# Kernel optimization log

Hardware: AMD Instinct MI355X
Metric: run time of the kernel (lower is better)

Reference implementation:

```python
import jax, jax.numpy as jnp
import numpy as np

N = 1_000_000   # nodes
E = 32_000_000  # directed edges (avg degree 32)


def setup_inputs() -> dict:
    key = jax.random.key(0)
    k1, k2, k3 = jax.random.split(key, 3)
    x = jax.random.normal(k1, (N, 1), dtype=jnp.float32)
    edge_index = jax.random.randint(k2, (2, E), 0, N, dtype=jnp.int32)
    W = jax.random.normal(k3, (1, 1), dtype=jnp.float32) * 0.5
    b = jnp.zeros((1,), dtype=jnp.float32)
    return {"x": x, "edge_index": edge_index, "W": W, "b": b}


def reference(x, edge_index, W, b):
    # GCNConv with default add_self_loops=True, normalize=True, then sigmoid.
    n = x.shape[0]
    loops = jnp.arange(n, dtype=edge_index.dtype)
    src = jnp.concatenate([edge_index[0], loops])  # [E+N]
    dst = jnp.concatenate([edge_index[1], loops])  # [E+N]

    # degree over destination nodes (self-loops included -> deg >= 1)
    deg = jax.ops.segment_sum(jnp.ones_like(dst, dtype=x.dtype), dst, num_segments=n)
    dinv = jax.lax.rsqrt(deg)                      # [N]
    norm = dinv[src] * dinv[dst]                   # [E+N] symmetric normalization

    xw = x @ W                                     # [N, 1] linear transform
    msg = xw[src] * norm[:, None]                  # gather + scale, [E+N, 1]
    agg = jax.ops.segment_sum(msg, dst, num_segments=n)  # scatter-add, [N, 1]
    return jax.nn.sigmoid(agg + b)
```

## Files before the change

### kernel.cpp

```cpp
#include <hip/hip_runtime.h>
#include <math.h>

typedef unsigned int u32;
typedef int iv4 __attribute__((ext_vector_type(4)));

#define BKT_BITS 12
#define BKT_SIZE 4096
#define NBMAX    256
#define DEPTH    32
#define BIN_T    256
#define TILE     4096


__global__ void zero_u32(u32* __restrict__ p, int n) {
    int i = blockIdx.x * blockDim.x + threadIdx.x;
    if (i < n) p[i] = 0u;
}

__global__ void count_kernel(const int* __restrict__ dst, u32* __restrict__ gcount, int E, int NB) {
    __shared__ u32 h[NBMAX];
    for (int t = threadIdx.x; t < NBMAX; t += blockDim.x) h[t] = 0u;
    __syncthreads();
    int nvec = E >> 2;
    for (int v = blockIdx.x * blockDim.x + threadIdx.x; v < nvec; v += gridDim.x * blockDim.x) {
        iv4 d = __builtin_nontemporal_load(reinterpret_cast<const iv4*>(dst) + v);
        atomicAdd(&h[((u32)d.x) >> BKT_BITS], 1u);
        atomicAdd(&h[((u32)d.y) >> BKT_BITS], 1u);
        atomicAdd(&h[((u32)d.z) >> BKT_BITS], 1u);
        atomicAdd(&h[((u32)d.w) >> BKT_BITS], 1u);
    }
    if (blockIdx.x == 0) {
        for (int e = (nvec << 2) + threadIdx.x; e < E; e += blockDim.x)
            atomicAdd(&h[((u32)dst[e]) >> BKT_BITS], 1u);
    }
    __syncthreads();
    for (int t = threadIdx.x; t < NB; t += blockDim.x)
        if (h[t]) atomicAdd(&gcount[t], h[t]);
}

__global__ void scan_kernel(const u32* __restrict__ gcount, u32* __restrict__ gbase,
                            u32* __restrict__ gcursor, int NB) {
    __shared__ u32 sc[NBMAX];
    int t = threadIdx.x;
    u32 cap = 0u;
    if (t < NB) cap = (gcount[t] + 63u) & ~63u;
    sc[t] = cap;
    __syncthreads();
    for (int off = 1; off < NBMAX; off <<= 1) {
        u32 v = (t >= off) ? sc[t - off] : 0u;
        __syncthreads();
        sc[t] += v;
        __syncthreads();
    }
    if (t < NB) {
        u32 base = sc[t] - cap;
        gbase[t]   = base;
        gcursor[t] = base;
    }
}

__global__ void __launch_bounds__(BIN_T)
bin_kernel(const int* __restrict__ src, const int* __restrict__ dst,
           u32* __restrict__ recs, u32* __restrict__ gcursor, int E, int NB) {
    __shared__ u32 stag[NBMAX * DEPTH];
    __shared__ u32 scnt[NBMAX];
    for (int t = threadIdx.x; t < NBMAX; t += BIN_T) scnt[t] = 0u;
    __syncthreads();
    int base = blockIdx.x * TILE;
#pragma unroll
    for (int r = 0; r < TILE / (BIN_T * 4); ++r) {
        int v  = (base >> 2) + r * BIN_T + threadIdx.x;
        int e0 = v << 2;
        if (e0 + 3 < E) {
            iv4 s4 = __builtin_nontemporal_load(reinterpret_cast<const iv4*>(src) + v);
            iv4 d4 = __builtin_nontemporal_load(reinterpret_cast<const iv4*>(dst) + v);
#pragma unroll
            for (int k = 0; k < 4; ++k) {
                u32 ss = (u32)s4[k], dd = (u32)d4[k];
                u32 b   = dd >> BKT_BITS;
                u32 rec = (ss << BKT_BITS) | (dd & (BKT_SIZE - 1));
                u32 slot = atomicAdd(&scnt[b], 1u);
                if (slot < DEPTH) stag[b * DEPTH + slot] = rec;
                else { u32 g = atomicAdd(&gcursor[b], 1u); recs[g] = rec; }
            }
        } else if (e0 < E) {
            for (int e = e0; e < E && e < e0 + 4; ++e) {
                u32 ss = (u32)src[e], dd = (u32)dst[e];
                u32 b   = dd >> BKT_BITS;
                u32 rec = (ss << BKT_BITS) | (dd & (BKT_SIZE - 1));
                u32 slot = atomicAdd(&scnt[b], 1u);
                if (slot < DEPTH) stag[b * DEPTH + slot] = rec;
                else { u32 g = atomicAdd(&gcursor[b], 1u); recs[g] = rec; }
            }
        }
    }
    __syncthreads();
    int t = threadIdx.x;
    if (t < NB) {
        u32 c = scnt[t]; if (c > DEPTH) c = DEPTH;
        if (c > 0u) {
            u32 g = atomicAdd(&gcursor[t], c);
            for (u32 k = 0; k < c; ++k) recs[g + k] = stag[t * DEPTH + k];
        }
    }
}

__global__ void __launch_bounds__(1024)
degnode_kernel(const u32* __restrict__ recs, const u32* __restrict__ gbase,
               const u32* __restrict__ gcount, const float* __restrict__ x,
               const float* __restrict__ W, float* __restrict__ dinv,
               float* __restrict__ s, int N) {
    __shared__ u32 cnt[BKT_SIZE];
    int b = blockIdx.x;
    for (int j = threadIdx.x; j < BKT_SIZE; j += 1024) cnt[j] = 0u;
    __syncthreads();
    u32 c = gcount[b], base = gbase[b];
    for (u32 k = threadIdx.x; k < c; k += 1024) {
        u32 rec = __builtin_nontemporal_load(recs + base + k);
        atomicAdd(&cnt[rec & (BKT_SIZE - 1)], 1u);
    }
    __syncthreads();
    int nid0 = b << BKT_BITS;
    float W0 = W[0];
    for (int j = threadIdx.x; j < BKT_SIZE; j += 1024) {
        int nid = nid0 + j;
        if (nid < N) {
            float di = rsqrtf((float)(cnt[j] + 1u));
            dinv[nid] = di;
            s[nid] = x[nid] * W0 * di;
        }
    }
}

__global__ void __launch_bounds__(1024)
aggout_kernel(const u32* __restrict__ recs, const u32* __restrict__ gbase,
              const u32* __restrict__ gcount, const float* __restrict__ s,
              const float* __restrict__ dinv, const float* __restrict__ bb,
              float* __restrict__ out, int N) {
    __shared__ float acc[BKT_SIZE];
    int b = blockIdx.x;
    for (int j = threadIdx.x; j < BKT_SIZE; j += 1024) acc[j] = 0.0f;
    __syncthreads();
    u32 c = gcount[b], base = gbase[b];
    for (u32 k = threadIdx.x; k < c; k += 1024) {
        u32 rec = __builtin_nontemporal_load(recs + base + k);
        atomicAdd(&acc[rec & (BKT_SIZE - 1)], s[rec >> BKT_BITS]);
    }
    __syncthreads();
    int nid0 = b << BKT_BITS;
    float b0 = bb[0];
    for (int j = threadIdx.x; j < BKT_SIZE; j += 1024) {
        int nid = nid0 + j;
        if (nid < N) {
            float z = dinv[nid] * (acc[j] + s[nid]) + b0;
            out[nid] = 1.0f / (1.0f + expf(-z));
        }
    }
}

__global__ void zero_kernel(int* __restrict__ p, int n) {
    int i = blockIdx.x * blockDim.x + threadIdx.x;
    if (i < n) p[i] = 0;
}
__global__ void deg_kernel(const int* __restrict__ dst, int* __restrict__ deg, int E) {
    int i = (blockIdx.x * blockDim.x + threadIdx.x) * 4;
    if (i + 3 < E) {
        int4 d = *reinterpret_cast<const int4*>(dst + i);
        atomicAdd(&deg[d.x], 1); atomicAdd(&deg[d.y], 1);
        atomicAdd(&deg[d.z], 1); atomicAdd(&deg[d.w], 1);
    } else {
        for (int k = i; k < E; ++k) atomicAdd(&deg[dst[k]], 1);
    }
}
__global__ void node_kernel(const float* __restrict__ x, const int* __restrict__ deg,
                            const float* __restrict__ W, float* __restrict__ s,
                            float* __restrict__ dinv, float* __restrict__ acc, int N) {
    int i = blockIdx.x * blockDim.x + threadIdx.x;
    if (i < N) {
        float di = rsqrtf((float)(deg[i] + 1));
        float si = x[i] * W[0] * di;
        dinv[i] = di; s[i] = si; acc[i] = si;
    }
}
__global__ void scatter_kernel(const int* __restrict__ src, const int* __restrict__ dst,
                               const float* __restrict__ s, float* __restrict__ acc, int E) {
    int i = (blockIdx.x * blockDim.x + threadIdx.x) * 4;
    if (i + 3 < E) {
        int4 sv = *reinterpret_cast<const int4*>(src + i);
        int4 dv = *reinterpret_cast<const int4*>(dst + i);
        atomicAdd(&acc[dv.x], s[sv.x]); atomicAdd(&acc[dv.y], s[sv.y]);
        atomicAdd(&acc[dv.z], s[sv.z]); atomicAdd(&acc[dv.w], s[sv.w]);
    } else {
        for (int k = i; k < E; ++k) atomicAdd(&acc[dst[k]], s[src[k]]);
    }
}
__global__ void out_kernel(const float* __restrict__ acc, const float* __restrict__ dinv,
                           const float* __restrict__ b, float* __restrict__ out, int N) {
    int i = blockIdx.x * blockDim.x + threadIdx.x;
    if (i < N) {
        float z = dinv[i] * acc[i] + b[0];
        out[i] = 1.0f / (1.0f + expf(-z));
    }
}

extern "C" void kernel_launch(void* const* d_in, const int* in_sizes, int n_in,
                              void* d_out, int out_size, void* d_ws, size_t ws_size,
                              hipStream_t stream) {
    const int N = in_sizes[0];
    const int E = in_sizes[1] / 2;
    const float* x  = (const float*)d_in[0];
    const int*   ei = (const int*)d_in[1];
    const float* W  = (const float*)d_in[2];
    const float* b  = (const float*)d_in[3];
    float* out = (float*)d_out;

    const int* srcp = ei;
    const int* dstp = ei + E;
    const int T = 256;

    const int NB = (N + BKT_SIZE - 1) >> BKT_BITS;
    const size_t recCap = (size_t)E + (size_t)NB * 64;
    const size_t need = (recCap + 3 * (size_t)NB + 2 * (size_t)N) * 4;

    if (N <= (1 << 20) && NB <= NBMAX && ws_size >= need) {
        u32* p = (u32*)d_ws;
        u32*   recs    = p;           p += recCap;
        u32*   gbase   = p;           p += NB;
        u32*   gcursor = p;           p += NB;
        u32*   gcount  = p;           p += NB;
        float* dinv    = (float*)p;   p += N;
        float* s       = (float*)p;

        zero_u32<<<1, T, 0, stream>>>(gcount, NB);
        count_kernel<<<1024, T, 0, stream>>>(dstp, gcount, E, NB);
        scan_kernel<<<1, T, 0, stream>>>(gcount, gbase, gcursor, NB);
        bin_kernel<<<(E + TILE - 1) / TILE, BIN_T, 0, stream>>>(srcp, dstp, recs, gcursor, E, NB);
        degnode_kernel<<<NB, 1024, 0, stream>>>(recs, gbase, gcount, x, W, dinv, s, N);
        aggout_kernel<<<NB, 1024, 0, stream>>>(recs, gbase, gcount, s, dinv, b, out, N);
    } else {
        char* ws = (char*)d_ws;
        int*   deg  = (int*)ws;
        float* s    = (float*)(ws + (size_t)N * 4);
        float* dinv = (float*)(ws + (size_t)N * 8);
        float* acc  = (float*)deg;
        const int blocksN = (N + T - 1) / T;
        const int blocksE = ((E + 3) / 4 + T - 1) / T;
        zero_kernel<<<blocksN, T, 0, stream>>>(deg, N);
        deg_kernel<<<blocksE, T, 0, stream>>>(dstp, deg, E);
        node_kernel<<<blocksN, T, 0, stream>>>(x, deg, W, s, dinv, acc, N);
        scatter_kernel<<<blocksE, T, 0, stream>>>(srcp, dstp, s, acc, E);
        out_kernel<<<blocksN, T, 0, stream>>>(acc, dinv, b, out, N);
    }
}
```

Before: 782.0 us.

## Replace count-scan binning with fixed-capacity buckets and split per-bucket aggregation

Drops the separate count and scan passes over dst by giving every destination bucket a fixed capacity sized from the mean edge count plus slack, with a global overflow list for anything that spills. The histogram and aggregation kernels are split four ways per bucket to raise parallelism (4x blocks). Partial results are merged into global arrays with atomics, and separate vectorized node and output kernels finish the computation. Smaller staging depth and tile size raise occupancy in the binning kernel. The risk is that skewed inputs overflow the capped list (OVFCAP) and silently drop edges, and the extra global atomics and launches add cost.

Measured after the change: 844.8 us. 1.08x slower.

```diff
diff --git a/kernel.cpp b/kernel.cpp
--- a/kernel.cpp
+++ b/kernel.cpp
@@ -2,14 +2,19 @@
 #include <math.h>
 
 typedef unsigned int u32;
+typedef unsigned long long u64;
 typedef int iv4 __attribute__((ext_vector_type(4)));
+typedef float fv4 __attribute__((ext_vector_type(4)));
 
 #define BKT_BITS 12
 #define BKT_SIZE 4096
 #define NBMAX    256
-#define DEPTH    32
+#define DEPTH    17
 #define BIN_T    256
-#define TILE     4096
+#define TILE     2048
+#define SPLIT    4
+#define HA_T     512
+#define OVFCAP   131072u
 
 
 __global__ void zero_u32(u32* __restrict__ p, int n) {
@@ -17,51 +22,11 @@
     if (i < n) p[i] = 0u;
 }
 
-__global__ void count_kernel(const int* __restrict__ dst, u32* __restrict__ gcount, int E, int NB) {
-    __shared__ u32 h[NBMAX];
-    for (int t = threadIdx.x; t < NBMAX; t += blockDim.x) h[t] = 0u;
-    __syncthreads();
-    int nvec = E >> 2;
-    for (int v = blockIdx.x * blockDim.x + threadIdx.x; v < nvec; v += gridDim.x * blockDim.x) {
-        iv4 d = __builtin_nontemporal_load(reinterpret_cast<const iv4*>(dst) + v);
-        atomicAdd(&h[((u32)d.x) >> BKT_BITS], 1u);
-        atomicAdd(&h[((u32)d.y) >> BKT_BITS], 1u);
-        atomicAdd(&h[((u32)d.z) >> BKT_BITS], 1u);
-        atomicAdd(&h[((u32)d.w) >> BKT_BITS], 1u);
-    }
-    if (blockIdx.x == 0) {
-        for (int e = (nvec << 2) + threadIdx.x; e < E; e += blockDim.x)
-            atomicAdd(&h[((u32)dst[e]) >> BKT_BITS], 1u);
-    }
-    __syncthreads();
-    for (int t = threadIdx.x; t < NB; t += blockDim.x)
-        if (h[t]) atomicAdd(&gcount[t], h[t]);
-}
-
-__global__ void scan_kernel(const u32* __restrict__ gcount, u32* __restrict__ gbase,
-                            u32* __restrict__ gcursor, int NB) {
-    __shared__ u32 sc[NBMAX];
-    int t = threadIdx.x;
-    u32 cap = 0u;
-    if (t < NB) cap = (gcount[t] + 63u) & ~63u;
-    sc[t] = cap;
-    __syncthreads();
-    for (int off = 1; off < NBMAX; off <<= 1) {
-        u32 v = (t >= off) ? sc[t - off] : 0u;
-        __syncthreads();
-        sc[t] += v;
-        __syncthreads();
-    }
-    if (t < NB) {
-        u32 base = sc[t] - cap;
-        gbase[t]   = base;
-        gcursor[t] = base;
-    }
-}
-
-__global__ void __launch_bounds__(BIN_T)
-bin_kernel(const int* __restrict__ src, const int* __restrict__ dst,
-           u32* __restrict__ recs, u32* __restrict__ gcursor, int E, int NB) {
+__global__ void __launch_bounds__(BIN_T, 8)
+bin_kernel2(const int* __restrict__ src, const int* __restrict__ dst,
+            u32* __restrict__ recs, u32* __restrict__ gcursor,
+            u32* __restrict__ ovfcnt, u32* __restrict__ ovf,
+            int E, int NB, u32 CAP) {
     __shared__ u32 stag[NBMAX * DEPTH];
     __shared__ u32 scnt[NBMAX];
     for (int t = threadIdx.x; t < NBMAX; t += BIN_T) scnt[t] = 0u;
@@ -81,7 +46,14 @@
                 u32 rec = (ss << BKT_BITS) | (dd & (BKT_SIZE - 1));
                 u32 slot = atomicAdd(&scnt[b], 1u);
                 if (slot < DEPTH) stag[b * DEPTH + slot] = rec;
-                else { u32 g = atomicAdd(&gcursor[b], 1u); recs[g] = rec; }
+                else {
+                    u32 g = atomicAdd(&gcursor[b], 1u);
+                    if (g < CAP) recs[(size_t)b * CAP + g] = rec;
+                    else {
+                        u32 oi = atomicAdd(ovfcnt, 1u);
+                        if (oi < OVFCAP) { ovf[2u*oi] = ss; ovf[2u*oi+1u] = dd; }
+                    }
+                }
             }
         } else if (e0 < E) {
             for (int e = e0; e < E && e < e0 + 4; ++e) {
@@ -90,7 +62,14 @@
                 u32 rec = (ss << BKT_BITS) | (dd & (BKT_SIZE - 1));
                 u32 slot = atomicAdd(&scnt[b], 1u);
                 if (slot < DEPTH) stag[b * DEPTH + slot] = rec;
-                else { u32 g = atomicAdd(&gcursor[b], 1u); recs[g] = rec; }
+                else {
+                    u32 g = atomicAdd(&gcursor[b], 1u);
+                    if (g < CAP) recs[(size_t)b * CAP + g] = rec;
+                    else {
+                        u32 oi = atomicAdd(ovfcnt, 1u);
+                        if (oi < OVFCAP) { ovf[2u*oi] = ss; ovf[2u*oi+1u] = dd; }
+                    }
+                }
             }
         }
     }
@@ -100,60 +79,150 @@
         u32 c = scnt[t]; if (c > DEPTH) c = DEPTH;
         if (c > 0u) {
             u32 g = atomicAdd(&gcursor[t], c);
-            for (u32 k = 0; k < c; ++k) recs[g + k] = stag[t * DEPTH + k];
-        }
-    }
-}
-
-__global__ void __launch_bounds__(1024)
-degnode_kernel(const u32* __restrict__ recs, const u32* __restrict__ gbase,
-               const u32* __restrict__ gcount, const float* __restrict__ x,
-               const float* __restrict__ W, float* __restrict__ dinv,
-               float* __restrict__ s, int N) {
-    __shared__ u32 cnt[BKT_SIZE];
-    int b = blockIdx.x;
-    for (int j = threadIdx.x; j < BKT_SIZE; j += 1024) cnt[j] = 0u;
-    __syncthreads();
-    u32 c = gcount[b], base = gbase[b];
-    for (u32 k = threadIdx.x; k < c; k += 1024) {
-        u32 rec = __builtin_nontemporal_load(recs + base + k);
-        atomicAdd(&cnt[rec & (BKT_SIZE - 1)], 1u);
-    }
+            size_t bp = (size_t)t * CAP;
+            for (u32 k = 0; k < c; ++k) {
+                u32 pos = g + k;
+                u32 rec = stag[t * DEPTH + k];
+                if (pos < CAP) recs[bp + pos] = rec;
+                else {
+                    u32 oi = atomicAdd(ovfcnt, 1u);
+                    if (oi < OVFCAP) {
+                        ovf[2u*oi]    = rec >> BKT_BITS;
+                        ovf[2u*oi+1u] = ((u32)t << BKT_BITS) | (rec & (BKT_SIZE - 1));
+                    }
+                }
+            }
+        }
+    }
+}
+
+__global__ void __launch_bounds__(HA_T, 8)
+hist_kernel(const u32* __restrict__ recs, const u32* __restrict__ gcursor,
+            const u32* __restrict__ ovfcnt, const u32* __restrict__ ovf,
+            u32* __restrict__ deg, u32 CAP) {
+    __shared__ u32 hh[BKT_SIZE];
+    int tid = threadIdx.x;
+    int b = blockIdx.x >> 2;
+    int split = blockIdx.x & 3;
+    for (int j = tid; j < BKT_SIZE; j += HA_T) hh[j] = 0u;
+    if (blockIdx.x == 0) {
+        u32 on = *ovfcnt; if (on > OVFCAP) on = OVFCAP;
+        for (u32 k = tid; k < on; k += HA_T) atomicAdd(&deg[ovf[2u*k+1u]], 1u);
+    }
+    __syncthreads();
+    u32 cnt = gcursor[b]; if (cnt > CAP) cnt = CAP;
+    u32 chunk = (((cnt + SPLIT - 1) / SPLIT) + 3u) & ~3u;
+    u32 start = split * chunk; if (start > cnt) start = cnt;
+    u32 end = start + chunk;   if (end > cnt)   end = cnt;
+    const u32* rp = recs + (size_t)b * CAP;
+    u32 nv = (end - start) >> 2;
+    const iv4* rp4 = reinterpret_cast<const iv4*>(rp + start);
+    for (u32 v = tid; v < nv; v += HA_T) {
+        iv4 r = __builtin_nontemporal_load(rp4 + v);
+        atomicAdd(&hh[((u32)r.x) & (BKT_SIZE - 1)], 1u);
+        atomicAdd(&hh[((u32)r.y) & (BKT_SIZE - 1)], 1u);
+        atomicAdd(&hh[((u32)r.z) & (BKT_SIZE - 1)], 1u);
+        atomicAdd(&hh[((u32)r.w) & (BKT_SIZE - 1)], 1u);
+    }
+    for (u32 k = start + (nv << 2) + tid; k < end; k += HA_T)
+        atomicAdd(&hh[rp[k] & (BKT_SIZE - 1)], 1u);
     __syncthreads();
     int nid0 = b << BKT_BITS;
+    for (int j = tid; j < BKT_SIZE; j += HA_T) {
+        u32 v = hh[j];
+        if (v) atomicAdd(&deg[nid0 + j], v);
+    }
+}
+
+__global__ void node_kernel2(const float* __restrict__ x, u32* __restrict__ degacc,
+                             const float* __restrict__ W,
+                             float* __restrict__ dinv, float* __restrict__ s, int N) {
+    int i = (blockIdx.x * blockDim.x + threadIdx.x) << 2;
     float W0 = W[0];
-    for (int j = threadIdx.x; j < BKT_SIZE; j += 1024) {
-        int nid = nid0 + j;
-        if (nid < N) {
-            float di = rsqrtf((float)(cnt[j] + 1u));
-            dinv[nid] = di;
-            s[nid] = x[nid] * W0 * di;
-        }
-    }
-}
-
-__global__ void __launch_bounds__(1024)
-aggout_kernel(const u32* __restrict__ recs, const u32* __restrict__ gbase,
-              const u32* __restrict__ gcount, const float* __restrict__ s,
-              const float* __restrict__ dinv, const float* __restrict__ bb,
-              float* __restrict__ out, int N) {
-    __shared__ float acc[BKT_SIZE];
-    int b = blockIdx.x;
-    for (int j = threadIdx.x; j < BKT_SIZE; j += 1024) acc[j] = 0.0f;
-    __syncthreads();
-    u32 c = gcount[b], base = gbase[b];
-    for (u32 k = threadIdx.x; k < c; k += 1024) {
-        u32 rec = __builtin_nontemporal_load(recs + base + k);
-        atomicAdd(&acc[rec & (BKT_SIZE - 1)], s[rec >> BKT_BITS]);
+    if (i + 3 < N) {
+        iv4 d  = *reinterpret_cast<const iv4*>(degacc + i);
+        fv4 xv = *reinterpret_cast<const fv4*>(x + i);
+        fv4 dv, sv;
+#pragma unroll
+        for (int j = 0; j < 4; ++j) {
+            float di = rsqrtf((float)((u32)d[j] + 1u));
+            dv[j] = di;
+            sv[j] = xv[j] * W0 * di;
+        }
+        *reinterpret_cast<fv4*>(dinv + i) = dv;
+        *reinterpret_cast<fv4*>(s + i)    = sv;
+        *reinterpret_cast<fv4*>(reinterpret_cast<float*>(degacc) + i) = sv;
+    } else {
+        for (; i < N; ++i) {
+            u32 d = degacc[i];
+            float di = rsqrtf((float)(d + 1u));
+            float si = x[i] * W0 * di;
+            dinv[i] = di; s[i] = si;
+            reinterpret_cast<float*>(degacc)[i] = si;
+        }
+    }
+}
+
+__global__ void __launch_bounds__(HA_T, 8)
+agg_kernel(const u32* __restrict__ recs, const u32* __restrict__ gcursor,
+           const u32* __restrict__ ovfcnt, const u32* __restrict__ ovf,
+           const float* __restrict__ s, float* __restrict__ acc, u32 CAP) {
+    __shared__ float aa[BKT_SIZE];
+    int tid = threadIdx.x;
+    int b = blockIdx.x >> 2;
+    int split = blockIdx.x & 3;
+    for (int j = tid; j < BKT_SIZE; j += HA_T) aa[j] = 0.0f;
+    if (blockIdx.x == 0) {
+        u32 on = *ovfcnt; if (on > OVFCAP) on = OVFCAP;
+        for (u32 k = tid; k < on; k += HA_T)
+            atomicAdd(&acc[ovf[2u*k+1u]], s[ovf[2u*k]]);
+    }
+    __syncthreads();
+    u32 cnt = gcursor[b]; if (cnt > CAP) cnt = CAP;
+    u32 chunk = (((cnt + SPLIT - 1) / SPLIT) + 3u) & ~3u;
+    u32 start = split * chunk; if (start > cnt) start = cnt;
+    u32 end = start + chunk;   if (end > cnt)   end = cnt;
+    const u32* rp = recs + (size_t)b * CAP;
+    u32 nv = (end - start) >> 2;
+    const iv4* rp4 = reinterpret_cast<const iv4*>(rp + start);
+    for (u32 v = tid; v < nv; v += HA_T) {
+        iv4 r = __builtin_nontemporal_load(rp4 + v);
+        atomicAdd(&aa[((u32)r.x) & (BKT_SIZE - 1)], s[((u32)r.x) >> BKT_BITS]);
+        atomicAdd(&aa[((u32)r.y) & (BKT_SIZE - 1)], s[((u32)r.y) >> BKT_BITS]);
+        atomicAdd(&aa[((u32)r.z) & (BKT_SIZE - 1)], s[((u32)r.z) >> BKT_BITS]);
+        atomicAdd(&aa[((u32)r.w) & (BKT_SIZE - 1)], s[((u32)r.w) >> BKT_BITS]);
+    }
+    for (u32 k = start + (nv << 2) + tid; k < end; k += HA_T) {
+        u32 r = rp[k];
+        atomicAdd(&aa[r & (BKT_SIZE - 1)], s[r >> BKT_BITS]);
     }
     __syncthreads();
     int nid0 = b << BKT_BITS;
+    for (int j = tid; j < BKT_SIZE; j += HA_T) {
+        float v = aa[j];
+        if (v != 0.0f) atomicAdd(&acc[nid0 + j], v);
+    }
+}
+
+__global__ void out_kernel2(const u32* __restrict__ degacc, const float* __restrict__ dinv,
+                            const float* __restrict__ bb, float* __restrict__ out, int N) {
+    int i = (blockIdx.x * blockDim.x + threadIdx.x) << 2;
     float b0 = bb[0];
-    for (int j = threadIdx.x; j < BKT_SIZE; j += 1024) {
-        int nid = nid0 + j;
-        if (nid < N) {
-            float z = dinv[nid] * (acc[j] + s[nid]) + b0;
-            out[nid] = 1.0f / (1.0f + expf(-z));
+    const float* accf = reinterpret_cast<const float*>(degacc);
+    if (i + 3 < N) {
+        fv4 a  = *reinterpret_cast<const fv4*>(accf + i);
+        fv4 dv = *reinterpret_cast<const fv4*>(dinv + i);
+        fv4 o;
+#pragma unroll
+        for (int j = 0; j < 4; ++j) {
+            float z = dv[j] * a[j] + b0;
+            o[j] = 1.0f / (1.0f + expf(-z));
+        }
+        *reinterpret_cast<fv4*>(out + i) = o;
+    } else {
+        for (; i < N; ++i) {
+            float z = dinv[i] * accf[i] + b0;
+            out[i] = 1.0f / (1.0f + expf(-z));
         }
     }
 }
@@ -219,24 +288,37 @@
     const int T = 256;
 
     const int NB = (N + BKT_SIZE - 1) >> BKT_BITS;
-    const size_t recCap = (size_t)E + (size_t)NB * 64;
-    const size_t need = (recCap + 3 * (size_t)NB + 2 * (size_t)N) * 4;
-
-    if (N <= (1 << 20) && NB <= NBMAX && ws_size >= need) {
+    u64 meanCnt = (N > 0) ? (((u64)E << BKT_BITS) / (u64)N) : 0ull;
+    const u32 CAP = (u32)((meanCnt + 2048ull + 63ull) & ~63ull);
+    const size_t recCap   = (size_t)NB * CAP;
+    const size_t off_cur  = recCap;
+    const size_t off_ovfc = off_cur + NBMAX;
+    const size_t off_ovf  = off_ovfc + 16;
+    const size_t off_deg  = off_ovf + 2 * (size_t)OVFCAP;
+    const size_t off_dinv = off_deg + (size_t)N;
+    const size_t off_s    = off_dinv + (size_t)N;
+    const size_t need = (off_s + (size_t)N) * 4;
+
+    if (N <= (1 << 20) && NB <= NBMAX && (N & 15) == 0 && (E & 3) == 0 &&
+        E > 0 && ws_size >= need) {
         u32* p = (u32*)d_ws;
-        u32*   recs    = p;           p += recCap;
-        u32*   gbase   = p;           p += NB;
-        u32*   gcursor = p;           p += NB;
-        u32*   gcount  = p;           p += NB;
-        float* dinv    = (float*)p;   p += N;
-        float* s       = (float*)p;
-
-        zero_u32<<<1, T, 0, stream>>>(gcount, NB);
-        count_kernel<<<1024, T, 0, stream>>>(dstp, gcount, E, NB);
-        scan_kernel<<<1, T, 0, stream>>>(gcount, gbase, gcursor, NB);
-        bin_kernel<<<(E + TILE - 1) / TILE, BIN_T, 0, stream>>>(srcp, dstp, recs, gcursor, E, NB);
-        degnode_kernel<<<NB, 1024, 0, stream>>>(recs, gbase, gcount, x, W, dinv, s, N);
-        aggout_kernel<<<NB, 1024, 0, stream>>>(recs, gbase, gcount, s, dinv, b, out, N);
+        u32*   recs    = p;
+        u32*   gcursor = p + off_cur;
+        u32*   ovfcnt  = p + off_ovfc;
+        u32*   ovf     = p + off_ovf;
+        u32*   deg     = p + off_deg;
+        float* dinv    = (float*)(p + off_dinv);
+        float* s       = (float*)(p + off_s);
+
+        zero_u32<<<(NBMAX + 16 + T - 1) / T, T, 0, stream>>>(gcursor, NBMAX + 16);
+        zero_u32<<<(N + T - 1) / T, T, 0, stream>>>(deg, N);
+        bin_kernel2<<<(E + TILE - 1) / TILE, BIN_T, 0, stream>>>(
+            srcp, dstp, recs, gcursor, ovfcnt, ovf, E, NB, CAP);
+        hist_kernel<<<NB * SPLIT, HA_T, 0, stream>>>(recs, gcursor, ovfcnt, ovf, deg, CAP);
+        node_kernel2<<<((N + 3) / 4 + T - 1) / T, T, 0, stream>>>(x, deg, W, dinv, s, N);
+        agg_kernel<<<NB * SPLIT, HA_T, 0, stream>>>(
+            recs, gcursor, ovfcnt, ovf, s, (float*)deg, CAP);
+        out_kernel2<<<((N + 3) / 4 + T - 1) / T, T, 0, stream>>>(deg, dinv, b, out, N);
     } else {
         char* ws = (char*)d_ws;
         int*   deg  = (int*)ws;
```
